# Kernel tuning notes

Measured on AMD Instinct MI355X. Metric: run time of the kernel, lower is better.

Reference implementation:

```python
import jax, jax.numpy as jnp
import numpy as np

B, S, D, H, V = 4, 1024, 1024, 16, 1024
HD = D // H  # head_dim = 64
FF = 4 * D


def _layer_norm(x, g, b, eps=1e-5):
    mu = jnp.mean(x, axis=-1, keepdims=True)
    var = jnp.var(x, axis=-1, keepdims=True)
    return (x - mu) * jax.lax.rsqrt(var + eps) * g + b


def _pos_encoding(seq_len, d_model):
    # sinusoidal PE, matching PositionalEncoding buffer construction
    pos = jnp.arange(seq_len, dtype=jnp.float32)[:, None]
    div = jnp.exp(jnp.arange(0, d_model, 2, dtype=jnp.float32) * (-np.log(10000.0) / d_model))
    pe = jnp.zeros((seq_len, d_model), dtype=jnp.float32)
    pe = pe.at[:, 0::2].set(jnp.sin(pos * div))
    pe = pe.at[:, 1::2].set(jnp.cos(pos * div))
    return pe


def setup_inputs() -> dict:
    key = jax.random.key(0)
    ks = jax.random.split(key, 12)
    sc = 0.02
    return {
        "inputs": jax.random.randint(ks[0], (B, S), 0, V, dtype=jnp.int32),
        "targets": jax.random.randint(ks[1], (B, S), 0, V, dtype=jnp.int32),
        "wte": jax.random.normal(ks[2], (V, D), jnp.float32) * sc,
        "wq": jax.random.normal(ks[3], (D, D), jnp.float32) * sc,
        "bq": jnp.zeros((D,), jnp.float32),
        "wk": jax.random.normal(ks[4], (D, D), jnp.float32) * sc,
        "bk": jnp.zeros((D,), jnp.float32),
        "wv": jax.random.normal(ks[5], (D, D), jnp.float32) * sc,
        "bv": jnp.zeros((D,), jnp.float32),
        "wo": jax.random.normal(ks[6], (D, D), jnp.float32) * sc,
        "bo": jnp.zeros((D,), jnp.float32),
        "w1": jax.random.normal(ks[7], (D, FF), jnp.float32) * sc,
        "b1": jnp.zeros((FF,), jnp.float32),
        "w2": jax.random.normal(ks[8], (FF, D), jnp.float32) * sc,
        "b2": jnp.zeros((D,), jnp.float32),
        "ln1_g": jnp.ones((D,), jnp.float32),
        "ln1_b": jnp.zeros((D,), jnp.float32),
        "ln2_g": jnp.ones((D,), jnp.float32),
        "ln2_b": jnp.zeros((D,), jnp.float32),
    }


def reference(inputs, targets, wte, wq, bq, wk, bk, wv, bv, wo, bo,
              w1, b1, w2, b2, ln1_g, ln1_b, ln2_g, ln2_b):
    # embedding + positional encoding
    x = wte[inputs] + _pos_encoding(S, D)  # [B,S,D]

    # naive causal multi-head attention (dropout = identity in eval)
    q = (x @ wq + bq).reshape(B, S, H, HD)
    k = (x @ wk + bk).reshape(B, S, H, HD)
    v = (x @ wv + bv).reshape(B, S, H, HD)
    scores = jnp.einsum('bqhd,bkhd->bhqk', q, k) / np.sqrt(HD)  # [B,H,S,S]
    causal = jnp.tril(jnp.ones((S, S), dtype=bool))
    scores = jnp.where(causal, scores, -jnp.inf)
    attn = jax.nn.softmax(scores, axis=-1)
    ctx = jnp.einsum('bhqk,bkhd->bqhd', attn, v).reshape(B, S, D)
    att_out = ctx @ wo + bo

    # residual + LN1, FFN + GELU, residual + LN2
    adn = _layer_norm(x + att_out, ln1_g, ln1_b)
    h = jax.nn.gelu(adn @ w1 + b1, approximate=False) @ w2 + b2
    logits = _layer_norm(h + adn, ln2_g, ln2_b)

    # cross-entropy over d_model(=vocab) classes
    logits_flat = logits.reshape(B * S, D)
    tgt = targets.reshape(B * S)
    logp = jax.nn.log_softmax(logits_flat, axis=-1)
    loss = -jnp.mean(jnp.take_along_axis(logp, tgt[:, None], axis=-1))
    return logits_flat, loss
```

## Files before the change

kernel.cpp:

```cpp
#include <hip/hip_runtime.h>
#include <math.h>

#define BB 4
#define SS 1024
#define DD 1024
#define HH 16
#define HDIM 64
#define FF 4096
#define MM 4096

typedef short bf16x8 __attribute__((ext_vector_type(8)));
typedef short bf16x4 __attribute__((ext_vector_type(4)));
typedef float f32x4  __attribute__((ext_vector_type(4)));

static __device__ __forceinline__ short f2bf(float f){
  unsigned u = __float_as_uint(f);
  u += 0x7FFFu + ((u >> 16) & 1u);
  return (short)(u >> 16);
}
static __device__ __forceinline__ float b2f(short s){
  return __uint_as_float(((unsigned)(unsigned short)s) << 16);
}

static __device__ __forceinline__ float erf_fast(float x){
  float ax = fabsf(x);
  float t  = __builtin_amdgcn_rcpf(1.0f + 0.3275911f * ax);
  float p  = t * (0.254829592f + t * (-0.284496736f + t * (1.421413741f +
             t * (-1.453152027f + t * 1.061405429f))));
  float e  = 1.0f - p * __expf(-ax * ax);
  return copysignf(e, x);
}

static __device__ __forceinline__ void gl_lds16(const short* g, short* l){
  __builtin_amdgcn_global_load_lds((const __attribute__((address_space(1))) unsigned int*)g,
                                   (__attribute__((address_space(3))) unsigned int*)l,
                                   16, 0, 0);
}

#define MFMA_BF16 __builtin_amdgcn_mfma_f32_16x16x32_bf16

__global__ __launch_bounds__(256) void trans_all_kernel(
    const float* __restrict__ wq, const float* __restrict__ wk,
    const float* __restrict__ wv, const float* __restrict__ wo,
    const float* __restrict__ w1, const float* __restrict__ w2,
    short* __restrict__ wqkvt, short* __restrict__ wot,
    short* __restrict__ w1t,   short* __restrict__ w2t){
  __shared__ float t[32][33];
  int idx = blockIdx.x;
  const float* src; short* dst; int R, C, cx, ry;
  if (idx < 4096){
    int wsel = idx >> 10, tt = idx & 1023;
    cx = tt & 31; ry = tt >> 5; R = 1024; C = 1024;
    src = (wsel == 0) ? wq : (wsel == 1) ? wk : (wsel == 2) ? wv : wo;
    dst = (wsel == 3) ? wot : wqkvt + (size_t)wsel * 1024 * 1024;
  } else if (idx < 8192){
    int tt = idx - 4096; cx = tt & 127; ry = tt >> 7; R = 1024; C = 4096;
    src = w1; dst = w1t;
  } else {
    int tt = idx - 8192; cx = tt & 31; ry = tt >> 5; R = 4096; C = 1024;
    src = w2; dst = w2t;
  }
  int c0 = cx * 32, r0 = ry * 32;
  int tx = threadIdx.x, ty = threadIdx.y;
#pragma unroll
  for (int i = 0; i < 32; i += 8)
    t[ty + i][tx] = src[(size_t)(r0 + ty + i) * C + (c0 + tx)];
  __syncthreads();
#pragma unroll
  for (int i = 0; i < 32; i += 8)
    dst[(size_t)(c0 + ty + i) * R + (r0 + tx)] = f2bf(t[tx][ty + i]);
}

__global__ __launch_bounds__(256) void concat_bias_kernel(const float* __restrict__ a,
                                                          const float* __restrict__ b,
                                                          const float* __restrict__ c,
                                                          float* __restrict__ dst){
  int t = blockIdx.x * 256 + threadIdx.x;
  float v = (t < 1024) ? a[t] : (t < 2048 ? b[t - 1024] : c[t - 2048]);
  dst[t] = v;
}

__global__ __launch_bounds__(256) void embed_kernel(const int* __restrict__ inputs,
                                                    const float* __restrict__ wte,
                                                    short* __restrict__ xb){
  int idx4 = blockIdx.x * 256 + threadIdx.x;
  int row = idx4 >> 8;
  int d   = (idx4 & 255) * 4;
  int s   = row & (SS - 1);
  int tok = inputs[row];
  float4 w = *(const float4*)&wte[(size_t)tok * DD + d];
  const float cdiv = -9.210340371976184f / 512.0f;
  int i0 = d >> 1;
  float ang0 = (float)s * expf((float)i0 * cdiv);
  float ang1 = (float)s * expf((float)(i0 + 1) * cdiv);
  float x0 = w.x + sinf(ang0);
  float x1 = w.y + cosf(ang0);
  float x2 = w.z + sinf(ang1);
  float x3 = w.w + cosf(ang1);
  bf16x4 sb; sb[0]=f2bf(x0); sb[1]=f2bf(x1); sb[2]=f2bf(x2); sb[3]=f2bf(x3);
  *(bf16x4*)&xb[(size_t)row * DD + d] = sb;
}

template<int MODE, bool GELU, bool ADDBIAS>
__global__ __launch_bounds__(512, 2) void gemm256_kernel(const short* __restrict__ A,
    const short* __restrict__ Bt, const float* __restrict__ bias,
    short* __restrict__ o0, short* __restrict__ o1,
    short* __restrict__ o2, short* __restrict__ o3,
    short* __restrict__ qo, short* __restrict__ ko, short* __restrict__ vto,
    int M, int N, int K, int Kc){
  __shared__ __align__(16) short lds[8 * 8192];
  int tid = threadIdx.x;
  int lid = blockIdx.y * gridDim.x + blockIdx.x;
  int cpx = (gridDim.x * gridDim.y) >> 3;
  int swz = (lid & 7) * cpx + (lid >> 3);
  int n0 = (swz % gridDim.x) * 256;
  int m0 = (swz / gridDim.x) * 256;
  int bz = blockIdx.z;
  int kbeg = bz * Kc;
  int w = tid >> 6, lane = tid & 63, lr = lane & 15, lg = lane >> 4;
  int wm = w >> 2, wn = w & 3;
  f32x4 acc[8][4] = {};

  int sr = lane >> 3;
  int sg = (lane & 7) ^ sr;
  auto STAGE_HALF = [&](int buf, int typ, int half, int kt){
    const short* s0 = (typ ? Bt : A) + (size_t)kbeg + sg * 8;
    int rb = (typ ? n0 : m0) + half * 128 + w * 8 + sr;
#pragma unroll
    for (int j = 0; j < 2; j++)
      gl_lds16(s0 + (size_t)(rb + j * 64) * K + kt * 64,
               &lds[(((buf << 2) | (typ << 1) | half) << 13) + (j << 12) + (w << 9)]);
  };

  int nt = Kc >> 6;
  STAGE_HALF(0, 0, 0, 0); STAGE_HALF(0, 0, 1, 0);
  STAGE_HALF(0, 1, 0, 0); STAGE_HALF(0, 1, 1, 0);
  STAGE_HALF(1, 0, 0, 1); STAGE_HALF(1, 0, 1, 1);
  STAGE_HALF(1, 1, 0, 1); STAGE_HALF(1, 1, 1, 1);
  asm volatile("s_waitcnt vmcnt(8)" ::: "memory");
  __builtin_amdgcn_s_barrier();

  int lr64 = lr * 64;
  int ck0 = ((lg     ) ^ (lr & 7)) * 8;
  int ck1 = ((lg + 4 ) ^ (lr & 7)) * 8;
  int brow = (wn & 1) << 12;

  bf16x8 Alo[4][2], Ahi[4][2], Blo[2][2], Bhi[2][2];

  for (int t = 0; t < nt; t++){
    int b = t & 1;
    int abase = (((b << 2) | wm) << 13) + lr64;
    int bbase = (((b << 2) | 2 | (wn >> 1)) << 13) + brow + lr64;

#pragma unroll
    for (int fi = 0; fi < 4; fi++){
      Alo[fi][0] = *(const bf16x8*)&lds[abase + fi * 1024 + ck0];
      Alo[fi][1] = *(const bf16x8*)&lds[abase + fi * 1024 + ck1];
    }
#pragma unroll
    for (int ni = 0; ni < 2; ni++){
      Blo[ni][0] = *(const bf16x8*)&lds[bbase + ni * 1024 + ck0];
      Blo[ni][1] = *(const bf16x8*)&lds[bbase + ni * 1024 + ck1];
    }
    __builtin_amdgcn_s_barrier();
    asm volatile("s_waitcnt lgkmcnt(0)" ::: "memory");
    __builtin_amdgcn_sched_barrier(0);
    __builtin_amdgcn_s_setprio(1);
#pragma unroll
    for (int mi = 0; mi < 4; mi++)
#pragma unroll
      for (int ni = 0; ni < 2; ni++){
        acc[mi][ni] = MFMA_BF16(Alo[mi][0], Blo[ni][0], acc[mi][ni], 0, 0, 0);
        acc[mi][ni] = MFMA_BF16(Alo[mi][1], Blo[ni][1], acc[mi][ni], 0, 0, 0);
      }
    __builtin_amdgcn_s_setprio(0);
    __builtin_amdgcn_s_barrier();

#pragma unroll
    for (int fi = 0; fi < 4; fi++){
      Ahi[fi][0] = *(const bf16x8*)&lds[abase + (fi + 4) * 1024 + ck0];
      Ahi[fi][1] = *(const bf16x8*)&lds[abase + (fi + 4) * 1024 + ck1];
    }
    __builtin_amdgcn_s_barrier();
    asm volatile("s_waitcnt lgkmcnt(0)" ::: "memory");
    __builtin_amdgcn_sched_barrier(0);
    __builtin_amdgcn_s_setprio(1);
#pragma unroll
    for (int mi = 0; mi < 4; mi++)
#pragma unroll
      for (int ni = 0; ni < 2; ni++){
        acc[mi + 4][ni] = MFMA_BF16(Ahi[mi][0], Blo[ni][0], acc[mi + 4][ni], 0, 0, 0);
        acc[mi + 4][ni] = MFMA_BF16(Ahi[mi][1], Blo[ni][1], acc[mi + 4][ni], 0, 0, 0);
      }
    __builtin_amdgcn_s_setprio(0);
    __builtin_amdgcn_s_barrier();

#pragma unroll
    for (int ni = 0; ni < 2; ni++){
      Bhi[ni][0] = *(const bf16x8*)&lds[bbase + (ni + 2) * 1024 + ck0];
      Bhi[ni][1] = *(const bf16x8*)&lds[bbase + (ni + 2) * 1024 + ck1];
    }
    if (t + 2 < nt){ STAGE_HALF(b, 0, 0, t + 2); STAGE_HALF(b, 0, 1, t + 2); }
    __builtin_amdgcn_s_barrier();
    asm volatile("s_waitcnt lgkmcnt(0)" ::: "memory");
    __builtin_amdgcn_sched_barrier(0);
    __builtin_amdgcn_s_setprio(1);
#pragma unroll
    for (int mi = 0; mi < 4; mi++)
#pragma unroll
      for (int ni = 0; ni < 2; ni++){
        acc[mi + 4][ni + 2] = MFMA_BF16(Ahi[mi][0], Bhi[ni][0], acc[mi + 4][ni + 2], 0, 0, 0);
        acc[mi + 4][ni + 2] = MFMA_BF16(Ahi[mi][1], Bhi[ni][1], acc[mi + 4][ni + 2], 0, 0, 0);
      }
    __builtin_amdgcn_s_setprio(0);
    __builtin_amdgcn_s_barrier();

    if (t + 2 < nt){ STAGE_HALF(b, 1, 0, t + 2); STAGE_HALF(b, 1, 1, t + 2); }
    __builtin_amdgcn_s_barrier();
    __builtin_amdgcn_sched_barrier(0);
    __builtin_amdgcn_s_setprio(1);
#pragma unroll
    for (int mi = 0; mi < 4; mi++)
#pragma unroll
      for (int ni = 0; ni < 2; ni++){
        acc[mi][ni + 2] = MFMA_BF16(Alo[mi][0], Bhi[ni][0], acc[mi][ni + 2], 0, 0, 0);
        acc[mi][ni + 2] = MFMA_BF16(Alo[mi][1], Bhi[ni][1], acc[mi][ni + 2], 0, 0, 0);
      }
    __builtin_amdgcn_s_setprio(0);
    if (t == nt - 2) asm volatile("s_waitcnt vmcnt(0)" ::: "memory");
    else             asm volatile("s_waitcnt vmcnt(8)" ::: "memory");
    __builtin_amdgcn_s_barrier();
  }

  short* slab = (MODE == 1) ? ((bz == 0) ? o0 : (bz == 1) ? o1 : (bz == 2) ? o2 : o3) : o0;
  bool addb = ADDBIAS && (MODE != 1 || bz == 0);
#pragma unroll
  for (int mi = 0; mi < 8; mi++){
#pragma unroll
    for (int ni = 0; ni < 4; ni++){
      int ng = n0 + wn * 64 + ni * 16 + lr;
      float bv = addb ? bias[ng] : 0.0f;
      int mg0 = m0 + wm * 128 + mi * 16 + 4 * lg;
      if (MODE == 2){
        int sel = n0 >> 10;
        if (sel == 2){
          int d = ng & 1023; int hh = d >> 6, nn = d & 63;
          int bI = mg0 >> 10, sI = mg0 & 1023;
          bf16x4 pk;
#pragma unroll
          for (int r = 0; r < 4; r++) pk[r] = f2bf(acc[mi][ni][r] + bv);
          *(bf16x4*)&vto[(((size_t)(bI * HH + hh)) * HDIM + nn) * SS + sI] = pk;
        } else {
          short* dst = (sel == 0) ? qo : ko;
#pragma unroll
          for (int r = 0; r < 4; r++)
            dst[(size_t)(mg0 + r) * DD + (ng & 1023)] = f2bf(acc[mi][ni][r] + bv);
        }
      } else {
#pragma unroll
        for (int r = 0; r < 4; r++){
          float v = acc[mi][ni][r] + bv;
          if (GELU) v = 0.5f * v * (1.0f + erf_fast(v * 0.70710678118654752f));
          slab[(size_t)(mg0 + r) * N + ng] = f2bf(v);
        }
      }
    }
  }
}

__global__ __launch_bounds__(256) void attn_kernel(const short* __restrict__ qb,
                                                   const short* __restrict__ kb,
                                                   const short* __restrict__ vtb,
                                                   short* __restrict__ ctxb){
  __shared__ __align__(16) short k_lds[2][64 * 64];
  __shared__ __align__(16) short v_lds[2][64 * 64];
  __shared__ __align__(16) short p_lds[4][2][16 * 72];
  int qp = blockIdx.x, h = blockIdx.y, b = blockIdx.z;
  int Tlo = qp, Thi = 15 - qp;
  int tid = threadIdx.x, w = tid >> 6, lane = tid & 63, lr = lane & 15, lg = lane >> 4;

  const short* kp0 = kb  + (size_t)b * SS * DD + h * HDIM;
  const short* vt0 = vtb + (size_t)(b * HH + h) * HDIM * SS;

  bf16x8 qf0[2], qf1[2];
#pragma unroll
  for (int ti = 0; ti < 2; ti++){
    int T = ti ? Thi : Tlo;
    const short* qp_ = qb + ((size_t)(b * SS + T * 64 + w * 16 + lr) * DD + h * HDIM);
    qf0[ti] = *(const bf16x8*)&qp_[lg * 8];
    qf1[ti] = *(const bf16x8*)&qp_[32 + lg * 8];
  }

  float m[2][4], l[2][4];
  f32x4 acc[2][4] = {};
#pragma unroll
  for (int ti = 0; ti < 2; ti++)
#pragma unroll
    for (int r = 0; r < 4; r++){ m[ti][r] = -1e30f; l[ti][r] = 0.0f; }

  int srow8 = lane >> 3;
  int sjs   = (lane & 7) ^ srow8;
  auto STAGE = [&](int buf, int kt){
#pragma unroll
    for (int i = 0; i < 2; i++){
      int rb  = (w + 4 * i) * 8;
      int row = rb + srow8;
      gl_lds16(kp0 + (size_t)(kt * 64 + row) * DD + sjs * 8, &k_lds[buf][rb * 64]);
      gl_lds16(vt0 + (size_t)row * SS + kt * 64 + sjs * 8,   &v_lds[buf][rb * 64]);
    }
  };

  int cur = 0;
  STAGE(0, 0);
  asm volatile("s_waitcnt vmcnt(0)" ::: "memory");
  __syncthreads();

  bf16x8 pf0[2], pf1[2];
  for (int kt = 0; kt <= Thi; kt++){
    if (kt < Thi) STAGE(cur ^ 1, kt + 1);

    bf16x8 kf0[4], kf1[4];
#pragma unroll
    for (int sub = 0; sub < 4; sub++){
      int r = sub * 16 + lr;
      kf0[sub] = *(const bf16x8*)&k_lds[cur][r * 64 + ((lg     ^ (r & 7)) * 8)];
      kf1[sub] = *(const bf16x8*)&k_lds[cur][r * 64 + (((lg+4) ^ (r & 7)) * 8)];
    }

#pragma unroll
    for (int ti = 0; ti < 2; ti++){
      int T = ti ? Thi : Tlo;
      if (kt > T) continue;
      f32x4 sc4[4];
#pragma unroll
      for (int sub = 0; sub < 4; sub++){
        f32x4 t = {};
        t = MFMA_BF16(qf0[ti], kf0[sub], t, 0, 0, 0);
        t = MFMA_BF16(qf1[ti], kf1[sub], t, 0, 0, 0);
#pragma unroll
        for (int r = 0; r < 4; r++) t[r] *= 0.125f;
        sc4[sub] = t;
      }
      if (kt == T){
#pragma unroll
        for (int sub = 0; sub < 4; sub++)
#pragma unroll
          for (int r = 0; r < 4; r++)
            if (16 * sub + lr > 16 * w + 4 * lg + r) sc4[sub][r] = -1e30f;
      }

      float pm[4];
#pragma unroll
      for (int r = 0; r < 4; r++)
        pm[r] = fmaxf(fmaxf(sc4[0][r], sc4[1][r]), fmaxf(sc4[2][r], sc4[3][r]));
#pragma unroll
      for (int off = 1; off < 16; off <<= 1)
#pragma unroll
        for (int r = 0; r < 4; r++) pm[r] = fmaxf(pm[r], __shfl_xor(pm[r], off));

      float scl[4], rs[4];
#pragma unroll
      for (int r = 0; r < 4; r++){
        float mn = fmaxf(m[ti][r], pm[r]);
        scl[r] = __expf(m[ti][r] - mn);
        m[ti][r] = mn;
        rs[r] = 0.0f;
      }
#pragma unroll
      for (int sub = 0; sub < 4; sub++)
#pragma unroll
        for (int r = 0; r < 4; r++){
          float p = __expf(sc4[sub][r] - m[ti][r]);
          sc4[sub][r] = p;
          rs[r] += p;
        }
#pragma unroll
      for (int off = 1; off < 16; off <<= 1)
#pragma unroll
        for (int r = 0; r < 4; r++) rs[r] += __shfl_xor(rs[r], off);
#pragma unroll
      for (int r = 0; r < 4; r++) l[ti][r] = l[ti][r] * scl[r] + rs[r];
#pragma unroll
      for (int nb = 0; nb < 4; nb++)
#pragma unroll
        for (int r = 0; r < 4; r++) acc[ti][nb][r] *= scl[r];

      short* pw = &p_lds[w][ti][0];
#pragma unroll
      for (int sub = 0; sub < 4; sub++)
#pragma unroll
        for (int r = 0; r < 4; r++)
          pw[(4 * lg + r) * 72 + sub * 16 + lr] = f2bf(sc4[sub][r]);
      pf0[ti] = *(const bf16x8*)&pw[lr * 72 + lg * 8];
      pf1[ti] = *(const bf16x8*)&pw[lr * 72 + 32 + lg * 8];
    }

    bf16x8 vf0[4], vf1[4];
#pragma unroll
    for (int nb = 0; nb < 4; nb++){
      int r = nb * 16 + lr;
      vf0[nb] = *(const bf16x8*)&v_lds[cur][r * 64 + ((lg     ^ (r & 7)) * 8)];
      vf1[nb] = *(const bf16x8*)&v_lds[cur][r * 64 + (((lg+4) ^ (r & 7)) * 8)];
    }

#pragma unroll
    for (int ti = 0; ti < 2; ti++){
      int T = ti ? Thi : Tlo;
      if (kt > T) continue;
#pragma unroll
      for (int nb = 0; nb < 4; nb++){
        acc[ti][nb] = MFMA_BF16(pf0[ti], vf0[nb], acc[ti][nb], 0, 0, 0);
        acc[ti][nb] = MFMA_BF16(pf1[ti], vf1[nb], acc[ti][nb], 0, 0, 0);
      }
    }

    asm volatile("s_waitcnt vmcnt(0)" ::: "memory");
    __syncthreads();
    cur ^= 1;
  }

#pragma unroll
  for (int ti = 0; ti < 2; ti++){
    int T = ti ? Thi : Tlo;
#pragma unroll
    for (int r = 0; r < 4; r++){
      float inv = 1.0f / l[ti][r];
      int row = T * 64 + w * 16 + 4 * lg + r;
#pragma unroll
      for (int nb = 0; nb < 4; nb++)
        ctxb[(size_t)(b * SS + row) * DD + h * HDIM + nb * 16 + lr] = f2bf(acc[ti][nb][r] * inv);
    }
  }
}

template<int NPART, bool WF32, bool LOSS>
__global__ __launch_bounds__(256) void ln_kernel(const short* __restrict__ p0,
                                                 const short* __restrict__ p1,
                                                 const short* __restrict__ p2,
                                                 const short* __restrict__ p3,
                                                 const short* __restrict__ resb,
                                                 const float* __restrict__ g,
                                                 const float* __restrict__ be,
                                                 float* __restrict__ of,
                                                 short* __restrict__ ob,
                                                 const int* __restrict__ tgt,
                                                 float* __restrict__ lrow){
  int row = blockIdx.x, tid = threadIdx.x;
  size_t base = (size_t)row * DD + tid * 4;
  bf16x4 rv = *(const bf16x4*)&resb[base];
  float x0 = b2f(rv[0]), x1 = b2f(rv[1]), x2 = b2f(rv[2]), x3 = b2f(rv[3]);
  const short* ps[4] = {p0, p1, p2, p3};
#pragma unroll
  for (int p = 0; p < NPART; p++){
    bf16x4 pv = *(const bf16x4*)&ps[p][base];
    x0 += b2f(pv[0]); x1 += b2f(pv[1]); x2 += b2f(pv[2]); x3 += b2f(pv[3]);
  }
  float s = x0 + x1 + x2 + x3;
  float q = x0 * x0 + x1 * x1 + x2 * x2 + x3 * x3;
#pragma unroll
  for (int off = 32; off; off >>= 1){ s += __shfl_xor(s, off); q += __shfl_xor(q, off); }
  __shared__ float red[9];
  if ((tid & 63) == 0){ red[tid >> 6] = s; red[4 + (tid >> 6)] = q; }
  __syncthreads();
  s = red[0] + red[1] + red[2] + red[3];
  q = red[4] + red[5] + red[6] + red[7];
  float mean = s * (1.0f / DD);
  float var  = q * (1.0f / DD) - mean * mean;
  float rstd = rsqrtf(var + 1e-5f);
  float4 gv  = *(const float4*)&g[tid * 4];
  float4 bev = *(const float4*)&be[tid * 4];
  float y0 = (x0 - mean) * rstd * gv.x + bev.x;
  float y1 = (x1 - mean) * rstd * gv.y + bev.y;
  float y2 = (x2 - mean) * rstd * gv.z + bev.z;
  float y3 = (x3 - mean) * rstd * gv.w + bev.w;
  if (WF32){
    *(float4*)&of[base] = make_float4(y0, y1, y2, y3);
  } else {
    bf16x4 sb; sb[0]=f2bf(y0); sb[1]=f2bf(y1); sb[2]=f2bf(y2); sb[3]=f2bf(y3);
    *(bf16x4*)&ob[base] = sb;
  }
  if (LOSS){
    __syncthreads();
    float mx = fmaxf(fmaxf(y0, y1), fmaxf(y2, y3));
#pragma unroll
    for (int off = 32; off; off >>= 1) mx = fmaxf(mx, __shfl_xor(mx, off));
    if ((tid & 63) == 0) red[tid >> 6] = mx;
    int t = tgt[row];
    if (tid == (t >> 2))
      red[8] = ((t & 3) == 0) ? y0 : ((t & 3) == 1) ? y1 : ((t & 3) == 2) ? y2 : y3;
    __syncthreads();
    mx = fmaxf(fmaxf(red[0], red[1]), fmaxf(red[2], red[3]));
    float se = __expf(y0 - mx) + __expf(y1 - mx) + __expf(y2 - mx) + __expf(y3 - mx);
#pragma unroll
    for (int off = 32; off; off >>= 1) se += __shfl_xor(se, off);
    if ((tid & 63) == 0) red[4 + (tid >> 6)] = se;
    __syncthreads();
    if (tid == 0){
      float tot = red[4] + red[5] + red[6] + red[7];
      lrow[row] = mx + logf(tot) - red[8];
    }
  }
}

__global__ __launch_bounds__(256) void loss_reduce_kernel(const float* __restrict__ pr,
                                                          float* __restrict__ outp){
  int tid = threadIdx.x;
  float s = 0.0f;
  for (int i = tid; i < MM; i += 256) s += pr[i];
#pragma unroll
  for (int off = 32; off; off >>= 1) s += __shfl_xor(s, off);
  __shared__ float red[4];
  if ((tid & 63) == 0) red[tid >> 6] = s;
  __syncthreads();
  if (tid == 0) outp[0] = (red[0] + red[1] + red[2] + red[3]) * (1.0f / MM);
}

extern "C" void kernel_launch(void* const* d_in, const int* in_sizes, int n_in,
                              void* d_out, int out_size, void* d_ws, size_t ws_size,
                              hipStream_t stream){
  const int*   inputs  = (const int*)  d_in[0];
  const int*   targets = (const int*)  d_in[1];
  const float* wte     = (const float*)d_in[2];
  const float* wq      = (const float*)d_in[3];
  const float* bq      = (const float*)d_in[4];
  const float* wk      = (const float*)d_in[5];
  const float* bk      = (const float*)d_in[6];
  const float* wv      = (const float*)d_in[7];
  const float* bvv     = (const float*)d_in[8];
  const float* wo      = (const float*)d_in[9];
  const float* bo      = (const float*)d_in[10];
  const float* w1      = (const float*)d_in[11];
  const float* b1      = (const float*)d_in[12];
  const float* w2      = (const float*)d_in[13];
  const float* b2      = (const float*)d_in[14];
  const float* ln1g    = (const float*)d_in[15];
  const float* ln1b    = (const float*)d_in[16];
  const float* ln2g    = (const float*)d_in[17];
  const float* ln2b    = (const float*)d_in[18];
  float* out = (float*)d_out;

  char* ws = (char*)d_ws;
  const size_t MB = 1024 * 1024;
  short* wqkvt = (short*)(ws + 0 * MB);
  short* wot   = (short*)(ws + 6 * MB);
  short* w1t   = (short*)(ws + 8 * MB);
  short* w2t   = (short*)(ws + 16 * MB);
  short* xb    = (short*)(ws + 24 * MB);
  short* qbuf  = (short*)(ws + 32 * MB);
  short* kbuf  = (short*)(ws + 40 * MB);
  short* vtb   = (short*)(ws + 48 * MB);
  short* ctxb  = (short*)(ws + 56 * MB);
  short* pr0   = (short*)(ws + 64 * MB);
  short* pr1   = (short*)(ws + 72 * MB);
  short* pr2   = (short*)(ws + 80 * MB);
  short* pr3   = (short*)(ws + 88 * MB);
  short* adnb  = (short*)(ws + 96 * MB);
  short* h1b   = (short*)(ws + 32 * MB);
  short* hs0   = (short*)(ws + 64 * MB);
  short* hs1   = (short*)(ws + 72 * MB);
  short* hs2   = (short*)(ws + 80 * MB);
  short* hs3   = (short*)(ws + 88 * MB);
  float* lrow  = (float*)(ws + 104 * MB);
  float* bqkv  = (float*)(ws + 105 * MB);

  trans_all_kernel<<<12288, dim3(32, 8), 0, stream>>>(
      wq, wk, wv, wo, w1, w2, wqkvt, wot, w1t, w2t);
  concat_bias_kernel<<<12, 256, 0, stream>>>(bq, bk, bvv, bqkv);

  embed_kernel<<<4096, 256, 0, stream>>>(inputs, wte, xb);

  gemm256_kernel<2, false, true><<<dim3(12, 16), 512, 0, stream>>>(
      xb, wqkvt, bqkv, nullptr, nullptr, nullptr, nullptr,
      qbuf, kbuf, vtb, MM, 3 * DD, DD, DD);

  attn_kernel<<<dim3(8, 16, 4), 256, 0, stream>>>(qbuf, kbuf, vtb, ctxb);

  gemm256_kernel<1, false, true><<<dim3(4, 16, 4), 512, 0, stream>>>(
      ctxb, wot, bo, pr0, pr1, pr2, pr3,
      nullptr, nullptr, nullptr, MM, DD, DD, 256);

  ln_kernel<4, false, false><<<4096, 256, 0, stream>>>(
      pr0, pr1, pr2, pr3, xb, ln1g, ln1b, nullptr, adnb, nullptr, nullptr);

  gemm256_kernel<0, true, true><<<dim3(16, 16), 512, 0, stream>>>(
      adnb, w1t, b1, h1b, nullptr, nullptr, nullptr,
      nullptr, nullptr, nullptr, MM, FF, DD, DD);

  gemm256_kernel<1, false, true><<<dim3(4, 16, 4), 512, 0, stream>>>(
      h1b, w2t, b2, hs0, hs1, hs2, hs3,
      nullptr, nullptr, nullptr, MM, DD, FF, 1024);

  ln_kernel<4, true, true><<<4096, 256, 0, stream>>>(
      hs0, hs1, hs2, hs3, adnb, ln2g, ln2b, out, nullptr, targets, lrow);

  loss_reduce_kernel<<<1, 256, 0, stream>>>(lrow, out + (size_t)MM * DD);
}
```

Baseline: 233.5 us.

## Software-pipeline LDS fragment reads across MFMA quadrants in GEMM main loop

Restructures the GEMM inner loop so LDS fragment loads for the next quadrant (and the next k-tile's Alo/Blo) are issued before the current MFMA block runs. Partial lgkmcnt waits replace full waits, which removes some barriers and lets LDS latency overlap with matrix math. Global staging is interleaved, with vmcnt waits placed differently. The tighter scheduling risks LDS read-after-write hazards across buffers and raises register pressure.

```diff
diff --git a/kernel.cpp b/kernel.cpp
--- a/kernel.cpp
+++ b/kernel.cpp
@@ -147,90 +147,62 @@
 
   bf16x8 Alo[4][2], Ahi[4][2], Blo[2][2], Bhi[2][2];
 
+#define ABASE(b) ((((b) << 2) | wm) << 13) + lr64
+#define BBASE(b) ((((b) << 2) | 2 | (wn >> 1)) << 13) + brow + lr64
+#define RD_ALO(b) { int ab_ = ABASE(b); _Pragma("unroll") for (int fi_ = 0; fi_ < 4; fi_++){ \
+    Alo[fi_][0] = *(const bf16x8*)&lds[ab_ + fi_ * 1024 + ck0]; \
+    Alo[fi_][1] = *(const bf16x8*)&lds[ab_ + fi_ * 1024 + ck1]; } }
+#define RD_AHI(b) { int ab_ = ABASE(b); _Pragma("unroll") for (int fi_ = 0; fi_ < 4; fi_++){ \
+    Ahi[fi_][0] = *(const bf16x8*)&lds[ab_ + (fi_ + 4) * 1024 + ck0]; \
+    Ahi[fi_][1] = *(const bf16x8*)&lds[ab_ + (fi_ + 4) * 1024 + ck1]; } }
+#define RD_BLO(b) { int bb_ = BBASE(b); _Pragma("unroll") for (int ni_ = 0; ni_ < 2; ni_++){ \
+    Blo[ni_][0] = *(const bf16x8*)&lds[bb_ + ni_ * 1024 + ck0]; \
+    Blo[ni_][1] = *(const bf16x8*)&lds[bb_ + ni_ * 1024 + ck1]; } }
+#define RD_BHI(b) { int bb_ = BBASE(b); _Pragma("unroll") for (int ni_ = 0; ni_ < 2; ni_++){ \
+    Bhi[ni_][0] = *(const bf16x8*)&lds[bb_ + (ni_ + 2) * 1024 + ck0]; \
+    Bhi[ni_][1] = *(const bf16x8*)&lds[bb_ + (ni_ + 2) * 1024 + ck1]; } }
+#define QUAD(MB, NB, AF, BF) \
+    __builtin_amdgcn_s_setprio(1); \
+    _Pragma("unroll") for (int mi_ = 0; mi_ < 4; mi_++) \
+      _Pragma("unroll") for (int ni_ = 0; ni_ < 2; ni_++){ \
+        acc[mi_ + MB][ni_ + NB] = MFMA_BF16(AF[mi_][0], BF[ni_][0], acc[mi_ + MB][ni_ + NB], 0, 0, 0); \
+        acc[mi_ + MB][ni_ + NB] = MFMA_BF16(AF[mi_][1], BF[ni_][1], acc[mi_ + MB][ni_ + NB], 0, 0, 0); } \
+    __builtin_amdgcn_s_setprio(0);
+
+  RD_ALO(0); RD_BLO(0);
+
   for (int t = 0; t < nt; t++){
-    int b = t & 1;
-    int abase = (((b << 2) | wm) << 13) + lr64;
-    int bbase = (((b << 2) | 2 | (wn >> 1)) << 13) + brow + lr64;
-
-#pragma unroll
-    for (int fi = 0; fi < 4; fi++){
-      Alo[fi][0] = *(const bf16x8*)&lds[abase + fi * 1024 + ck0];
-      Alo[fi][1] = *(const bf16x8*)&lds[abase + fi * 1024 + ck1];
-    }
-#pragma unroll
-    for (int ni = 0; ni < 2; ni++){
-      Blo[ni][0] = *(const bf16x8*)&lds[bbase + ni * 1024 + ck0];
-      Blo[ni][1] = *(const bf16x8*)&lds[bbase + ni * 1024 + ck1];
-    }
+    int b = t & 1, bn = b ^ 1;
+    RD_AHI(b);
+    asm volatile("s_waitcnt lgkmcnt(8)" ::: "memory");
+    __builtin_amdgcn_sched_barrier(0);
+    QUAD(0, 0, Alo, Blo);
     __builtin_amdgcn_s_barrier();
+    RD_BHI(b);
+    if (t + 2 < nt){ STAGE_HALF(b, 0, 0, t + 2); STAGE_HALF(b, 0, 1, t + 2); }
+    asm volatile("s_waitcnt lgkmcnt(4)" ::: "memory");
+    __builtin_amdgcn_sched_barrier(0);
+    QUAD(4, 0, Ahi, Blo);
+    __builtin_amdgcn_s_barrier();
+    if (t + 2 < nt) asm volatile("s_waitcnt vmcnt(4)" ::: "memory");
+    else            asm volatile("s_waitcnt vmcnt(0)" ::: "memory");
+    if (t + 2 < nt){ STAGE_HALF(b, 1, 0, t + 2); STAGE_HALF(b, 1, 1, t + 2); }
     asm volatile("s_waitcnt lgkmcnt(0)" ::: "memory");
     __builtin_amdgcn_sched_barrier(0);
-    __builtin_amdgcn_s_setprio(1);
-#pragma unroll
-    for (int mi = 0; mi < 4; mi++)
-#pragma unroll
-      for (int ni = 0; ni < 2; ni++){
-        acc[mi][ni] = MFMA_BF16(Alo[mi][0], Blo[ni][0], acc[mi][ni], 0, 0, 0);
-        acc[mi][ni] = MFMA_BF16(Alo[mi][1], Blo[ni][1], acc[mi][ni], 0, 0, 0);
-      }
-    __builtin_amdgcn_s_setprio(0);
+    QUAD(4, 2, Ahi, Bhi);
     __builtin_amdgcn_s_barrier();
-
-#pragma unroll
-    for (int fi = 0; fi < 4; fi++){
-      Ahi[fi][0] = *(const bf16x8*)&lds[abase + (fi + 4) * 1024 + ck0];
-      Ahi[fi][1] = *(const bf16x8*)&lds[abase + (fi + 4) * 1024 + ck1];
-    }
+    QUAD(0, 2, Alo, Bhi);
+    __builtin_amdgcn_sched_barrier(0);
+    if (t + 1 < nt){ RD_ALO(bn); RD_BLO(bn); }
     __builtin_amdgcn_s_barrier();
-    asm volatile("s_waitcnt lgkmcnt(0)" ::: "memory");
-    __builtin_amdgcn_sched_barrier(0);
-    __builtin_amdgcn_s_setprio(1);
-#pragma unroll
-    for (int mi = 0; mi < 4; mi++)
-#pragma unroll
-      for (int ni = 0; ni < 2; ni++){
-        acc[mi + 4][ni] = MFMA_BF16(Ahi[mi][0], Blo[ni][0], acc[mi + 4][ni], 0, 0, 0);
-        acc[mi + 4][ni] = MFMA_BF16(Ahi[mi][1], Blo[ni][1], acc[mi + 4][ni], 0, 0, 0);
-      }
-    __builtin_amdgcn_s_setprio(0);
-    __builtin_amdgcn_s_barrier();
-
-#pragma unroll
-    for (int ni = 0; ni < 2; ni++){
-      Bhi[ni][0] = *(const bf16x8*)&lds[bbase + (ni + 2) * 1024 + ck0];
-      Bhi[ni][1] = *(const bf16x8*)&lds[bbase + (ni + 2) * 1024 + ck1];
-    }
-    if (t + 2 < nt){ STAGE_HALF(b, 0, 0, t + 2); STAGE_HALF(b, 0, 1, t + 2); }
-    __builtin_amdgcn_s_barrier();
-    asm volatile("s_waitcnt lgkmcnt(0)" ::: "memory");
-    __builtin_amdgcn_sched_barrier(0);
-    __builtin_amdgcn_s_setprio(1);
-#pragma unroll
-    for (int mi = 0; mi < 4; mi++)
-#pragma unroll
-      for (int ni = 0; ni < 2; ni++){
-        acc[mi + 4][ni + 2] = MFMA_BF16(Ahi[mi][0], Bhi[ni][0], acc[mi + 4][ni + 2], 0, 0, 0);
-        acc[mi + 4][ni + 2] = MFMA_BF16(Ahi[mi][1], Bhi[ni][1], acc[mi + 4][ni + 2], 0, 0, 0);
-      }
-    __builtin_amdgcn_s_setprio(0);
-    __builtin_amdgcn_s_barrier();
-
-    if (t + 2 < nt){ STAGE_HALF(b, 1, 0, t + 2); STAGE_HALF(b, 1, 1, t + 2); }
-    __builtin_amdgcn_s_barrier();
-    __builtin_amdgcn_sched_barrier(0);
-    __builtin_amdgcn_s_setprio(1);
-#pragma unroll
-    for (int mi = 0; mi < 4; mi++)
-#pragma unroll
-      for (int ni = 0; ni < 2; ni++){
-        acc[mi][ni + 2] = MFMA_BF16(Alo[mi][0], Bhi[ni][0], acc[mi][ni + 2], 0, 0, 0);
-        acc[mi][ni + 2] = MFMA_BF16(Alo[mi][1], Bhi[ni][1], acc[mi][ni + 2], 0, 0, 0);
-      }
-    __builtin_amdgcn_s_setprio(0);
-    if (t == nt - 2) asm volatile("s_waitcnt vmcnt(0)" ::: "memory");
-    else             asm volatile("s_waitcnt vmcnt(8)" ::: "memory");
-    __builtin_amdgcn_s_barrier();
-  }
+  }
+#undef QUAD
+#undef RD_BHI
+#undef RD_BLO
+#undef RD_AHI
+#undef RD_ALO
+#undef BBASE
+#undef ABASE
 
   short* slab = (MODE == 1) ? ((bz == 0) ? o0 : (bz == 1) ? o1 : (bz == 2) ? o2 : o3) : o0;
   bool addb = ADDBIAS && (MODE != 1 || bz == 0);
```

Result: faster. 225.7 us (-3.3%).
